# Kernel tuning notes

Hardware: AMD Instinct MI355X
Metric: run time of the kernel (lower is better)

The kernel has to match this reference:

```python
import jax, jax.numpy as jnp
import numpy as np

H = 16      # n_head
DK = 64     # d_k = n_feat // n_head
EPS = 1e-5  # nn.LayerNorm default eps


def _layernorm(x, gamma, beta):
    # LayerNorm over the last (d_k) dim, matching nn.LayerNorm(d_k)
    mu = jnp.mean(x, axis=-1, keepdims=True)
    var = jnp.mean(jnp.square(x - mu), axis=-1, keepdims=True)
    return (x - mu) * jax.lax.rsqrt(var + EPS) * gamma + beta


def setup_inputs() -> dict:
    key = jax.random.key(0)
    ks = jax.random.split(key, 10)
    B, T, D = 4, 1024, 1024
    s = 0.02
    inp = {
        "query": jax.random.normal(ks[0], (B, T, D), dtype=jnp.float32),
        "key":   jax.random.normal(ks[1], (B, T, D), dtype=jnp.float32),
        "value": jax.random.normal(ks[2], (B, T, D), dtype=jnp.float32),
        "mask":  jax.random.randint(ks[3], (B, T, T), 0, 2).astype(bool),
        # projection weights (torch nn.Linear: y = x @ W.T + b)
        "Wq": jax.random.normal(ks[4], (D, D), dtype=jnp.float32) * s,
        "bq": jnp.zeros((D,), dtype=jnp.float32),
        "Wk": jax.random.normal(ks[5], (D, D), dtype=jnp.float32) * s,
        "bk": jnp.zeros((D,), dtype=jnp.float32),
        "Wv": jax.random.normal(ks[6], (D, D), dtype=jnp.float32) * s,
        "bv": jnp.zeros((D,), dtype=jnp.float32),
        "Wo": jax.random.normal(ks[7], (D, D), dtype=jnp.float32) * s,
        "bo": jnp.zeros((D,), dtype=jnp.float32),
        # per-head LayerNorm params over d_k
        "q_gamma": jnp.ones((DK,), dtype=jnp.float32),
        "q_beta":  jnp.zeros((DK,), dtype=jnp.float32),
        "k_gamma": jnp.ones((DK,), dtype=jnp.float32),
        "k_beta":  jnp.zeros((DK,), dtype=jnp.float32),
    }
    return inp


def reference(query, key, value, mask, Wq, bq, Wk, bk, Wv, bv, Wo, bo,
              q_gamma, q_beta, k_gamma, k_beta):
    B, Tq, D = query.shape
    Tk = key.shape[1]
    # forward_qkv: project, split heads, QK-LayerNorm
    q = (query @ Wq.T + bq).reshape(B, Tq, H, DK)
    k = (key   @ Wk.T + bk).reshape(B, Tk, H, DK)
    q = _layernorm(q, q_gamma, q_beta).transpose(0, 2, 1, 3)  # (B,H,Tq,dk)
    k = _layernorm(k, k_gamma, k_beta).transpose(0, 2, 1, 3)  # (B,H,Tk,dk)
    v = (value @ Wv.T + bv).reshape(B, Tk, H, DK).transpose(0, 2, 1, 3)
    # scores scaled by sqrt(d_k)
    scores = jnp.einsum('bhqd,bhkd->bhqk', q, k) / jnp.sqrt(jnp.float32(DK))
    m = mask[:, None]  # (B,1,Tq,Tk) broadcast over heads
    scores = jnp.where(m, jnp.float32(-10000.0), scores)
    attn = jax.nn.softmax(scores, axis=-1)
    attn = jnp.where(m, jnp.float32(0.0), attn)
    # dropout is identity (p=0.0, eval)
    x = jnp.einsum('bhqk,bhkd->bhqd', attn, v)
    x = x.transpose(0, 2, 1, 3).reshape(B, Tq, H * DK)
    return x @ Wo.T + bo
```

## Files before the change

kernel.cpp:

```cpp
#include <hip/hip_runtime.h>
#include <cstdint>
#include <cstddef>

typedef _Float16 half8  __attribute__((ext_vector_type(8)));
typedef _Float16 half4v __attribute__((ext_vector_type(4)));
typedef float    f32x4  __attribute__((ext_vector_type(4)));

__device__ __forceinline__ f32x4 fzero4() {
  f32x4 v; v[0] = v[1] = v[2] = v[3] = 0.0f; return v;
}

__device__ __forceinline__ void gload16(const void* g, void* l) {
  __builtin_amdgcn_global_load_lds(
      (const __attribute__((address_space(1))) unsigned int*)g,
      (__attribute__((address_space(3))) unsigned int*)l, 16, 0, 0);
}

#define MFMA(a, b, c) __builtin_amdgcn_mfma_f32_16x16x32_f16(a, b, c, 0, 0, 0)
#define EXP2(x) __builtin_amdgcn_exp2f(x)

__device__ __forceinline__ float row16_sum(float x) {
#define STEP_(N)                                                         \
  {                                                                      \
    int t_ = __builtin_amdgcn_update_dpp(0, __float_as_int(x), 0x120 | N, \
                                         0xf, 0xf, true);                \
    x = x + __int_as_float(t_);                                          \
  }
  STEP_(8) STEP_(4) STEP_(2) STEP_(1)
#undef STEP_
  return x;
}

struct PrepArgs {
  const float* src[7];
  _Float16*    dst[7];
  const int*   mask;
  unsigned long long* mbits;
};

__global__ __launch_bounds__(256) void prep_kernel(PrepArgs a) {
  const int z = blockIdx.y;
  const int nthr = gridDim.x * blockDim.x;
  const int t0 = blockIdx.x * blockDim.x + threadIdx.x;
  if (z < 3) {
    const float4* __restrict__ s = (const float4*)a.src[z];
    half4v* __restrict__ d = (half4v*)a.dst[z];
    float4 v[8];
#pragma unroll
    for (int k = 0; k < 8; ++k) v[k] = s[t0 + k * nthr];
#pragma unroll
    for (int k = 0; k < 8; ++k) {
      half4v h;
      h[0] = (_Float16)v[k].x; h[1] = (_Float16)v[k].y;
      h[2] = (_Float16)v[k].z; h[3] = (_Float16)v[k].w;
      d[t0 + k * nthr] = h;
    }
  } else if (z < 7) {
    const float4* __restrict__ s = (const float4*)a.src[z];
    half4v* __restrict__ d = (half4v*)a.dst[z];
    float4 v[2];
#pragma unroll
    for (int k = 0; k < 2; ++k) v[k] = s[t0 + k * nthr];
#pragma unroll
    for (int k = 0; k < 2; ++k) {
      half4v h;
      h[0] = (_Float16)v[k].x; h[1] = (_Float16)v[k].y;
      h[2] = (_Float16)v[k].z; h[3] = (_Float16)v[k].w;
      d[t0 + k * nthr] = h;
    }
  } else {
    const int* __restrict__ src = a.mask;
    const unsigned char* __restrict__ s8 = (const unsigned char*)src;
    unsigned long long* __restrict__ dst = a.mbits;
    const int lane = threadIdx.x & 63;
    unsigned probe = 0;
#pragma unroll
    for (int e = 0; e < 16; ++e) probe |= s8[4 * (lane * 16 + e) + 1];
    const bool isbool = __any(probe != 0);

    const int gw = blockIdx.x * 4 + (threadIdx.x >> 6);
    for (int ii = 0; ii < 32; ii += 8) {
      int mv[8];
#pragma unroll
      for (int k = 0; k < 8; ++k) {
        const int word = gw * 32 + ii + k;
        const int t = word & 1023;
        const int kw = (word >> 10) & 15;
        const int b = word >> 14;
        const size_t idx = ((size_t)(b * 1024 + t)) * 1024 + kw * 64 + lane;
        mv[k] = isbool ? (int)s8[idx] : src[idx];
      }
#pragma unroll
      for (int k = 0; k < 8; ++k) {
        unsigned long long bal = __ballot(mv[k] != 0);
        if (lane == 0) dst[gw * 32 + ii + k] = bal;
      }
    }
  }
}

#define SM_SCALE 0.18033688011112042f

__global__ __launch_bounds__(256) void proj_kernel(
    const _Float16* __restrict__ q16, const _Float16* __restrict__ k16,
    const _Float16* __restrict__ v16, const _Float16* __restrict__ w16,
    const float* __restrict__ bq, const float* __restrict__ bk,
    const float* __restrict__ bv,
    const float* __restrict__ qg, const float* __restrict__ qbt,
    const float* __restrict__ kg, const float* __restrict__ kbt,
    _Float16* __restrict__ Qln, _Float16* __restrict__ Kln,
    _Float16* __restrict__ VT) {
  __shared__ _Float16 As[2][128 * 32];
  __shared__ _Float16 Bs[2][128 * 32];

  const int tid = threadIdx.x;
  const int w = tid >> 6, lane = tid & 63, g = lane >> 4, l15 = lane & 15;
  const int flat = blockIdx.x;
  const int swz = (flat & 7) * 96 + (flat >> 3);
  const int bn = swz & 7;
  const int bm = (swz >> 3) & 31;
  const int z = swz >> 8;

  const _Float16* A = (z == 0) ? q16 : ((z == 1) ? k16 : v16);
  const _Float16* W = w16 + (size_t)z * (1024 * 1024);
  const float* bias = (z == 0) ? bq : ((z == 1) ? bk : bv);

  const int wr = w >> 1, wc = w & 1;
  const int lrow16 = lane >> 2;
  const int csw = (((lane & 3) ^ ((lane >> 3) & 3)) << 3);
  const int rslot = (l15 >> 1) & 3;

  f32x4 acc[4][4];
#pragma unroll
  for (int i = 0; i < 4; ++i)
#pragma unroll
    for (int j = 0; j < 4; ++j) acc[i][j] = fzero4();

#define PROJ_STAGE(KT, BUF)                                                 \
  _Pragma("unroll") for (int c = 0; c < 2; ++c) {                           \
    const int row0 = w * 32 + c * 16;                                       \
    gload16(A + (size_t)(bm * 128 + row0 + lrow16) * 1024 + (KT)*32 + csw,  \
            &As[BUF][row0 * 32]);                                           \
    gload16(W + (size_t)(bn * 128 + row0 + lrow16) * 1024 + (KT)*32 + csw,  \
            &Bs[BUF][row0 * 32]);                                           \
  }

#define PROJ_TILE(KT, CUR, NXT, PF)                                         \
  {                                                                         \
    if (PF) { PROJ_STAGE((KT) + 1, NXT) }                                   \
    half8 a[4], b[4];                                                       \
    _Pragma("unroll") for (int mi = 0; mi < 4; ++mi) a[mi] =                \
        *(const half8*)&As[CUR][(wr * 64 + mi * 16 + l15) * 32 +            \
                                ((g ^ rslot) << 3)];                        \
    _Pragma("unroll") for (int nj = 0; nj < 4; ++nj) b[nj] =                \
        *(const half8*)&Bs[CUR][(wc * 64 + nj * 16 + l15) * 32 +            \
                                ((g ^ rslot) << 3)];                        \
    __builtin_amdgcn_s_setprio(1);                                          \
    _Pragma("unroll") for (int mi = 0; mi < 4; ++mi)                        \
        _Pragma("unroll") for (int nj = 0; nj < 4; ++nj) acc[mi][nj] =      \
            MFMA(a[mi], b[nj], acc[mi][nj]);                                \
    __builtin_amdgcn_s_setprio(0);                                          \
    if (PF) {                                                               \
      asm volatile("s_waitcnt vmcnt(0)" ::: "memory");                      \
      __syncthreads();                                                      \
    }                                                                       \
  }

  PROJ_STAGE(0, 0)
  asm volatile("s_waitcnt vmcnt(0)" ::: "memory");
  __syncthreads();
  for (int kt = 0; kt < 32; kt += 2) {
    PROJ_TILE(kt, 0, 1, true);
    PROJ_TILE(kt + 1, 1, 0, (kt + 1) < 31);
  }
#undef PROJ_TILE
#undef PROJ_STAGE

  const int colbase = bn * 128 + wc * 64;
  const int h = colbase >> 6;
  const int rowbase = bm * 128 + wr * 64;

  float biasv[4];
#pragma unroll
  for (int nj = 0; nj < 4; ++nj) biasv[nj] = bias[colbase + nj * 16 + l15];

  if (z < 2) {
    const float* gamma = (z == 0) ? qg : kg;
    const float* beta = (z == 0) ? qbt : kbt;
    const float sc = (z == 0) ? SM_SCALE : 1.0f;
    _Float16* dst = (z == 0) ? Qln : Kln;
    float gam[4], bet[4];
#pragma unroll
    for (int nj = 0; nj < 4; ++nj) {
      gam[nj] = gamma[nj * 16 + l15] * sc;
      bet[nj] = beta[nj * 16 + l15] * sc;
    }
#pragma unroll
    for (int mi = 0; mi < 4; ++mi) {
#pragma unroll
      for (int j = 0; j < 4; ++j) {
        float vals[4], s = 0.f, s2 = 0.f;
#pragma unroll
        for (int nj = 0; nj < 4; ++nj) {
          float v = acc[mi][nj][j] + biasv[nj];
          vals[nj] = v; s += v; s2 += v * v;
        }
        s = row16_sum(s);
        s2 = row16_sum(s2);
        const float mu = s * (1.0f / 64.0f);
        const float var = s2 * (1.0f / 64.0f) - mu * mu;
        const float rs = rsqrtf(var + 1e-5f);
        const int r = rowbase + mi * 16 + g * 4 + j;
        const int b = r >> 10, t = r & 1023;
        _Float16* drow = dst + ((size_t)((b * 16 + h) * 1024 + t)) * 64;
#pragma unroll
        for (int nj = 0; nj < 4; ++nj)
          drow[nj * 16 + l15] =
              (_Float16)((vals[nj] - mu) * rs * gam[nj] + bet[nj]);
      }
    }
  } else {
#pragma unroll
    for (int mi = 0; mi < 4; ++mi) {
      const int r0 = rowbase + mi * 16 + g * 4;
      const int b = r0 >> 10, t0 = r0 & 1023;
#pragma unroll
      for (int nj = 0; nj < 4; ++nj) {
        const int dk = nj * 16 + l15;
        half4v pk;
#pragma unroll
        for (int j = 0; j < 4; ++j)
          pk[j] = (_Float16)(acc[mi][nj][j] + biasv[nj]);
        *(half4v*)&VT[((size_t)((b * 16 + h) * 64 + dk)) * 1024 + t0] = pk;
      }
    }
  }
}

#define PSTR 76

__global__ __launch_bounds__(512) void attn_kernel(
    const _Float16* __restrict__ Qln, const _Float16* __restrict__ Kln,
    const _Float16* __restrict__ VT,
    const unsigned long long* __restrict__ mbits, _Float16* __restrict__ X) {
  __shared__ _Float16 PQ[128 * PSTR];
  __shared__ _Float16 Ks[2][64 * 64];
  __shared__ _Float16 Vs[2][64 * 64];
  __shared__ unsigned long long Mb[2][128];

  const int tid = threadIdx.x;
  const int w = tid >> 6, lane = tid & 63, g = lane >> 4, l15 = lane & 15;
  const int qt = blockIdx.x;
  const int bh = blockIdx.y;
  const int b = bh >> 4, h = bh & 15;

  const int lr8 = lane >> 3;
  const int csw = ((lane & 7) ^ lr8) << 3;

  const _Float16* Qb = Qln + (size_t)bh * 65536;
  const _Float16* Kb = Kln + (size_t)bh * 65536;
  const _Float16* Vb = VT + (size_t)bh * 65536;
  const unsigned long long* mbb = mbits + (size_t)b * 16384 + qt * 128;

  gload16(Qb + (size_t)(qt * 128 + w * 16 + lr8) * 64 + csw, &PQ[(w * 16) * 64]);
  gload16(Qb + (size_t)(qt * 128 + w * 16 + 8 + lr8) * 64 + csw,
          &PQ[(w * 16 + 8) * 64]);
  gload16(Kb + (size_t)(w * 8 + lr8) * 64 + csw, &Ks[0][(w * 8) * 64]);
  gload16(Vb + (size_t)(w * 8 + lr8) * 1024 + csw, &Vs[0][(w * 8) * 64]);
  if (w == 0) gload16(mbb + lane * 2, &Mb[0][0]);
  asm volatile("s_waitcnt vmcnt(0)" ::: "memory");
  __syncthreads();

  const int rsw = (l15 & 7) << 3;
  half8 qf[2];
#pragma unroll
  for (int kk = 0; kk < 2; ++kk)
    qf[kk] = *(const half8*)&PQ[(w * 16 + l15) * 64 + ((kk * 32 + g * 8) ^ rsw)];
  asm volatile("s_waitcnt lgkmcnt(0)" ::: "memory");
  __syncthreads();

  f32x4 o[4];
  float lsum[4];
#pragma unroll
  for (int dn = 0; dn < 4; ++dn) o[dn] = fzero4();
#pragma unroll
  for (int j = 0; j < 4; ++j) lsum[j] = 0.f;

#define ATTN_TILE(KT, CUR, NXT, PF)                                          \
  {                                                                          \
    if (PF) {                                                                \
      gload16(Kb + (size_t)(((KT) + 1) * 64 + w * 8 + lr8) * 64 + csw,       \
              &Ks[NXT][(w * 8) * 64]);                                       \
      gload16(Vb + (size_t)(w * 8 + lr8) * 1024 + ((KT) + 1) * 64 + csw,     \
              &Vs[NXT][(w * 8) * 64]);                                       \
      if (w == 0)                                                            \
        gload16(mbb + (size_t)((KT) + 1) * 1024 + lane * 2, &Mb[NXT][0]);    \
    }                                                                        \
    f32x4 s[4];                                                              \
    _Pragma("unroll") for (int nj = 0; nj < 4; ++nj) s[nj] = fzero4();       \
    _Pragma("unroll") for (int kk = 0; kk < 2; ++kk) {                       \
      half8 qv = qf[kk];                                                     \
      __builtin_amdgcn_s_setprio(1);                                         \
      _Pragma("unroll") for (int nj = 0; nj < 4; ++nj) {                     \
        half8 kf = *(const half8*)&Ks[CUR][(nj * 16 + l15) * 64 +            \
                                          ((kk * 32 + g * 8) ^ rsw)];        \
        s[nj] = MFMA(qv, kf, s[nj]);                                         \
      }                                                                      \
      __builtin_amdgcn_s_setprio(0);                                         \
    }                                                                        \
    _Pragma("unroll") for (int j = 0; j < 4; ++j) {                          \
      const int lrow = w * 16 + g * 4 + j;                                   \
      const unsigned long long mw = Mb[CUR][lrow];                           \
      const unsigned lo = (unsigned)mw, hi = (unsigned)(mw >> 32);           \
      const float p0 = ((lo >> l15) & 1) ? 0.f : EXP2(s[0][j]);              \
      const float p1 = ((lo >> (l15 + 16)) & 1) ? 0.f : EXP2(s[1][j]);       \
      const float p2 = ((hi >> l15) & 1) ? 0.f : EXP2(s[2][j]);              \
      const float p3 = ((hi >> (l15 + 16)) & 1) ? 0.f : EXP2(s[3][j]);       \
      PQ[lrow * PSTR + 0 + l15] = (_Float16)p0;                              \
      PQ[lrow * PSTR + 16 + l15] = (_Float16)p1;                             \
      PQ[lrow * PSTR + 32 + l15] = (_Float16)p2;                             \
      PQ[lrow * PSTR + 48 + l15] = (_Float16)p3;                             \
      lsum[j] += (p0 + p1) + (p2 + p3);                                      \
    }                                                                        \
    _Pragma("unroll") for (int kk = 0; kk < 2; ++kk) {                       \
      half8 pa = *(const half8*)&PQ[(w * 16 + l15) * PSTR + kk * 32 + g * 8];\
      __builtin_amdgcn_s_setprio(1);                                         \
      _Pragma("unroll") for (int dn = 0; dn < 4; ++dn) {                     \
        half8 vf = *(const half8*)&Vs[CUR][(dn * 16 + l15) * 64 +            \
                                           ((kk * 32 + g * 8) ^ rsw)];       \
        o[dn] = MFMA(pa, vf, o[dn]);                                         \
      }                                                                      \
      __builtin_amdgcn_s_setprio(0);                                         \
    }                                                                        \
    if (PF) {                                                                \
      asm volatile("s_waitcnt vmcnt(0)" ::: "memory");                       \
      __syncthreads();                                                       \
    }                                                                        \
  }

  for (int kt = 0; kt < 16; kt += 2) {
    ATTN_TILE(kt, 0, 1, true);
    ATTN_TILE(kt + 1, 1, 0, (kt + 1) < 15);
  }
#undef ATTN_TILE

#pragma unroll
  for (int j = 0; j < 4; ++j) {
    const int t = qt * 128 + w * 16 + g * 4 + j;
    const float inv = 1.0f / row16_sum(lsum[j]);
    _Float16* xrow = X + ((size_t)(b * 1024 + t)) * 1024 + h * 64;
#pragma unroll
    for (int dn = 0; dn < 4; ++dn)
      xrow[dn * 16 + l15] = (_Float16)(o[dn][j] * inv);
  }
}

__global__ __launch_bounds__(512) void ogemm_kernel(
    const _Float16* __restrict__ Xin, const _Float16* __restrict__ Wo16,
    const float* __restrict__ bo, float* __restrict__ out) {
  __shared__ _Float16 As[2][128 * 32];
  __shared__ _Float16 Bs[2][128 * 32];

  const int tid = threadIdx.x;
  const int w = tid >> 6, lane = tid & 63, g = lane >> 4, l15 = lane & 15;
  const int flat = blockIdx.x;
  const int swz = (flat & 7) * 32 + (flat >> 3);
  const int bn = swz & 7;
  const int bm = swz >> 3;
  const int wr = w >> 2, wc = w & 3;
  const int lrow16 = lane >> 2;
  const int csw = (((lane & 3) ^ ((lane >> 3) & 3)) << 3);
  const int rslot = (l15 >> 1) & 3;

  f32x4 acc[4][2];
#pragma unroll
  for (int i = 0; i < 4; ++i)
#pragma unroll
    for (int j = 0; j < 2; ++j) acc[i][j] = fzero4();

#define OG_STAGE(KT, BUF)                                                   \
  {                                                                         \
    const int row0 = w * 16;                                                \
    gload16(Xin + (size_t)(bm * 128 + row0 + lrow16) * 1024 + (KT)*32 + csw,\
            &As[BUF][row0 * 32]);                                           \
    gload16(Wo16 + (size_t)(bn * 128 + row0 + lrow16) * 1024 + (KT)*32 +    \
                csw,                                                        \
            &Bs[BUF][row0 * 32]);                                           \
  }

#define OG_TILE(KT, CUR, NXT, PF)                                           \
  {                                                                         \
    if (PF) { OG_STAGE((KT) + 1, NXT) }                                     \
    half8 a[4], b[2];                                                       \
    _Pragma("unroll") for (int mi = 0; mi < 4; ++mi) a[mi] =                \
        *(const half8*)&As[CUR][(wr * 64 + mi * 16 + l15) * 32 +            \
                                ((g ^ rslot) << 3)];                        \
    _Pragma("unroll") for (int nj = 0; nj < 2; ++nj) b[nj] =                \
        *(const half8*)&Bs[CUR][(wc * 32 + nj * 16 + l15) * 32 +            \
                                ((g ^ rslot) << 3)];                        \
    __builtin_amdgcn_s_setprio(1);                                          \
    _Pragma("unroll") for (int mi = 0; mi < 4; ++mi)                        \
        _Pragma("unroll") for (int nj = 0; nj < 2; ++nj) acc[mi][nj] =      \
            MFMA(a[mi], b[nj], acc[mi][nj]);                                \
    __builtin_amdgcn_s_setprio(0);                                          \
    if (PF) {                                                               \
      asm volatile("s_waitcnt vmcnt(0)" ::: "memory");                      \
      __syncthreads();                                                      \
    }                                                                       \
  }

  OG_STAGE(0, 0)
  asm volatile("s_waitcnt vmcnt(0)" ::: "memory");
  __syncthreads();
  for (int kt = 0; kt < 32; kt += 2) {
    OG_TILE(kt, 0, 1, true);
    OG_TILE(kt + 1, 1, 0, (kt + 1) < 31);
  }
#undef OG_TILE
#undef OG_STAGE

  const int colbase = bn * 128 + wc * 32;
  const int rowbase = bm * 128 + wr * 64;
  float biasv[2];
#pragma unroll
  for (int nj = 0; nj < 2; ++nj) biasv[nj] = bo[colbase + nj * 16 + l15];
#pragma unroll
  for (int mi = 0; mi < 4; ++mi)
#pragma unroll
    for (int nj = 0; nj < 2; ++nj)
#pragma unroll
      for (int j = 0; j < 4; ++j) {
        const int r = rowbase + mi * 16 + g * 4 + j;
        out[(size_t)r * 1024 + colbase + nj * 16 + l15] =
            acc[mi][nj][j] + biasv[nj];
      }
}

extern "C" void kernel_launch(void* const* d_in, const int* in_sizes, int n_in,
                              void* d_out, int out_size, void* d_ws,
                              size_t ws_size, hipStream_t stream) {
  const float* query = (const float*)d_in[0];
  const float* key = (const float*)d_in[1];
  const float* value = (const float*)d_in[2];
  const int* mask = (const int*)d_in[3];
  const float* Wq = (const float*)d_in[4];
  const float* bq = (const float*)d_in[5];
  const float* Wk = (const float*)d_in[6];
  const float* bk = (const float*)d_in[7];
  const float* Wv = (const float*)d_in[8];
  const float* bv = (const float*)d_in[9];
  const float* Wo = (const float*)d_in[10];
  const float* bo = (const float*)d_in[11];
  const float* qg = (const float*)d_in[12];
  const float* qb = (const float*)d_in[13];
  const float* kg = (const float*)d_in[14];
  const float* kb = (const float*)d_in[15];
  float* out = (float*)d_out;

  const size_t M4 = (size_t)4 * 1024 * 1024;
  const size_t M1 = (size_t)1024 * 1024;
  _Float16* q16 = (_Float16*)d_ws;
  _Float16* k16 = q16 + M4;
  _Float16* v16 = k16 + M4;
  _Float16* w16 = v16 + M4;
  _Float16* Qln = w16 + M4;
  _Float16* Kln = Qln + M4;
  _Float16* VTp = Kln + M4;
  _Float16* X = VTp + M4;
  unsigned long long* mbits = (unsigned long long*)(X + M4);

  PrepArgs pa;
  pa.src[0] = query; pa.src[1] = key; pa.src[2] = value;
  pa.src[3] = Wq; pa.src[4] = Wk; pa.src[5] = Wv; pa.src[6] = Wo;
  pa.dst[0] = q16; pa.dst[1] = k16; pa.dst[2] = v16;
  pa.dst[3] = w16; pa.dst[4] = w16 + M1; pa.dst[5] = w16 + 2 * M1;
  pa.dst[6] = w16 + 3 * M1;
  pa.mask = mask;
  pa.mbits = mbits;

  prep_kernel<<<dim3(512, 8), 256, 0, stream>>>(pa);
  proj_kernel<<<dim3(768), 256, 0, stream>>>(
      q16, k16, v16, w16, bq, bk, bv, qg, qb, kg, kb, Qln, Kln, VTp);
  attn_kernel<<<dim3(8, 64), 512, 0, stream>>>(Qln, Kln, VTp, mbits, X);
  ogemm_kernel<<<dim3(256), 512, 0, stream>>>(X, w16 + 3 * M1, bo, out);
}
```

Baseline: 130.3 us.

## Triple-buffer GEMM K-loops with partial vmcnt waits and retile output GEMM

Both projection GEMMs move from double buffering with full vmcnt(0) drains to a three-stage LDS ring that keeps one tile of loads in flight, using partial waitcnt and raw s_barrier. The output GEMM is retiled to 128x64 tiles with a K-step of 64, 256 threads and 512 blocks, using a new XOR swizzle. The attention grid is transposed so consecutive blocks walk across batch-heads rather than query tiles. This trades more LDS per block for better overlap of global loads with MFMA work and better occupancy in the last GEMM.

```diff
diff --git a/kernel.cpp b/kernel.cpp
--- a/kernel.cpp
+++ b/kernel.cpp
@@ -18,6 +18,8 @@
 
 #define MFMA(a, b, c) __builtin_amdgcn_mfma_f32_16x16x32_f16(a, b, c, 0, 0, 0)
 #define EXP2(x) __builtin_amdgcn_exp2f(x)
+#define WAITV(N) asm volatile("s_waitcnt vmcnt(" #N ")" ::: "memory")
+#define BAR() __builtin_amdgcn_s_barrier()
 
 __device__ __forceinline__ float row16_sum(float x) {
 #define STEP_(N)                                                         \
@@ -110,8 +112,8 @@
     const float* __restrict__ kg, const float* __restrict__ kbt,
     _Float16* __restrict__ Qln, _Float16* __restrict__ Kln,
     _Float16* __restrict__ VT) {
-  __shared__ _Float16 As[2][128 * 32];
-  __shared__ _Float16 Bs[2][128 * 32];
+  __shared__ _Float16 As[3][128 * 32];
+  __shared__ _Float16 Bs[3][128 * 32];
 
   const int tid = threadIdx.x;
   const int w = tid >> 6, lane = tid & 63, g = lane >> 4, l15 = lane & 15;
@@ -145,9 +147,8 @@
             &Bs[BUF][row0 * 32]);                                           \
   }
 
-#define PROJ_TILE(KT, CUR, NXT, PF)                                         \
+#define PROJ_COMP(CUR)                                                      \
   {                                                                         \
-    if (PF) { PROJ_STAGE((KT) + 1, NXT) }                                   \
     half8 a[4], b[4];                                                       \
     _Pragma("unroll") for (int mi = 0; mi < 4; ++mi) a[mi] =                \
         *(const half8*)&As[CUR][(wr * 64 + mi * 16 + l15) * 32 +            \
@@ -160,20 +161,22 @@
         _Pragma("unroll") for (int nj = 0; nj < 4; ++nj) acc[mi][nj] =      \
             MFMA(a[mi], b[nj], acc[mi][nj]);                                \
     __builtin_amdgcn_s_setprio(0);                                          \
-    if (PF) {                                                               \
-      asm volatile("s_waitcnt vmcnt(0)" ::: "memory");                      \
-      __syncthreads();                                                      \
-    }                                                                       \
   }
 
   PROJ_STAGE(0, 0)
-  asm volatile("s_waitcnt vmcnt(0)" ::: "memory");
-  __syncthreads();
-  for (int kt = 0; kt < 32; kt += 2) {
-    PROJ_TILE(kt, 0, 1, true);
-    PROJ_TILE(kt + 1, 1, 0, (kt + 1) < 31);
-  }
-#undef PROJ_TILE
+  PROJ_STAGE(1, 1)
+  WAITV(4);
+  BAR();
+  for (int t = 0; t < 30; t += 3) {
+    PROJ_STAGE(t + 2, 2) PROJ_COMP(0) WAITV(4); BAR();
+    PROJ_STAGE(t + 3, 0) PROJ_COMP(1) WAITV(4); BAR();
+    PROJ_STAGE(t + 4, 1) PROJ_COMP(2) WAITV(4); BAR();
+  }
+  PROJ_COMP(0)
+  WAITV(0);
+  BAR();
+  PROJ_COMP(1)
+#undef PROJ_COMP
 #undef PROJ_STAGE
 
   const int colbase = bn * 128 + wc * 64;
@@ -250,8 +253,8 @@
 
   const int tid = threadIdx.x;
   const int w = tid >> 6, lane = tid & 63, g = lane >> 4, l15 = lane & 15;
-  const int qt = blockIdx.x;
-  const int bh = blockIdx.y;
+  const int qt = blockIdx.y;
+  const int bh = blockIdx.x;
   const int b = bh >> 4, h = bh & 15;
 
   const int lr8 = lane >> 3;
@@ -355,22 +358,23 @@
   }
 }
 
-__global__ __launch_bounds__(512) void ogemm_kernel(
+__global__ __launch_bounds__(256) void ogemm_kernel(
     const _Float16* __restrict__ Xin, const _Float16* __restrict__ Wo16,
     const float* __restrict__ bo, float* __restrict__ out) {
-  __shared__ _Float16 As[2][128 * 32];
-  __shared__ _Float16 Bs[2][128 * 32];
+  __shared__ _Float16 As[3][128 * 64];
+  __shared__ _Float16 Bs[3][64 * 64];
 
   const int tid = threadIdx.x;
   const int w = tid >> 6, lane = tid & 63, g = lane >> 4, l15 = lane & 15;
   const int flat = blockIdx.x;
-  const int swz = (flat & 7) * 32 + (flat >> 3);
-  const int bn = swz & 7;
-  const int bm = swz >> 3;
-  const int wr = w >> 2, wc = w & 3;
-  const int lrow16 = lane >> 2;
-  const int csw = (((lane & 3) ^ ((lane >> 3) & 3)) << 3);
-  const int rslot = (l15 >> 1) & 3;
+  const int swz = (flat & 7) * 64 + (flat >> 3);
+  const int bn = swz & 15;
+  const int bm = swz >> 4;
+  const int wr = w >> 1, wc = w & 1;
+  const int srow = (w << 3) + (lane >> 3);
+  const int lr8 = lane >> 3;
+  const int csw = ((lane & 7) ^ lr8) << 3;
+  const int rsw = (l15 & 7) << 3;
 
   f32x4 acc[4][2];
 #pragma unroll
@@ -380,46 +384,51 @@
 
 #define OG_STAGE(KT, BUF)                                                   \
   {                                                                         \
-    const int row0 = w * 16;                                                \
-    gload16(Xin + (size_t)(bm * 128 + row0 + lrow16) * 1024 + (KT)*32 + csw,\
-            &As[BUF][row0 * 32]);                                           \
-    gload16(Wo16 + (size_t)(bn * 128 + row0 + lrow16) * 1024 + (KT)*32 +    \
-                csw,                                                        \
-            &Bs[BUF][row0 * 32]);                                           \
-  }
-
-#define OG_TILE(KT, CUR, NXT, PF)                                           \
-  {                                                                         \
-    if (PF) { OG_STAGE((KT) + 1, NXT) }                                     \
+    _Pragma("unroll") for (int r = 0; r < 4; ++r) {                         \
+      gload16(Xin + (size_t)(bm * 128 + r * 32 + srow) * 1024 + (KT)*64 +   \
+                  csw,                                                      \
+              &As[BUF][(r * 32 + (w << 3)) * 64]);                          \
+    }                                                                       \
+    _Pragma("unroll") for (int c = 0; c < 2; ++c) {                         \
+      gload16(Wo16 + (size_t)(bn * 64 + w * 16 + c * 8 + lr8) * 1024 +      \
+                  (KT)*64 + csw,                                            \
+              &Bs[BUF][(w * 16 + c * 8) * 64]);                             \
+    }                                                                       \
+  }
+
+#define OG_COMP(CUR)                                                        \
+  _Pragma("unroll") for (int kk = 0; kk < 2; ++kk) {                        \
     half8 a[4], b[2];                                                       \
     _Pragma("unroll") for (int mi = 0; mi < 4; ++mi) a[mi] =                \
-        *(const half8*)&As[CUR][(wr * 64 + mi * 16 + l15) * 32 +            \
-                                ((g ^ rslot) << 3)];                        \
+        *(const half8*)&As[CUR][(wr * 64 + mi * 16 + l15) * 64 +            \
+                                ((kk * 32 + g * 8) ^ rsw)];                 \
     _Pragma("unroll") for (int nj = 0; nj < 2; ++nj) b[nj] =                \
-        *(const half8*)&Bs[CUR][(wc * 32 + nj * 16 + l15) * 32 +            \
-                                ((g ^ rslot) << 3)];                        \
+        *(const half8*)&Bs[CUR][(wc * 32 + nj * 16 + l15) * 64 +            \
+                                ((kk * 32 + g * 8) ^ rsw)];                 \
     __builtin_amdgcn_s_setprio(1);                                          \
     _Pragma("unroll") for (int mi = 0; mi < 4; ++mi)                        \
         _Pragma("unroll") for (int nj = 0; nj < 2; ++nj) acc[mi][nj] =      \
             MFMA(a[mi], b[nj], acc[mi][nj]);                                \
     __builtin_amdgcn_s_setprio(0);                                          \
-    if (PF) {                                                               \
-      asm volatile("s_waitcnt vmcnt(0)" ::: "memory");                      \
-      __syncthreads();                                                      \
-    }                                                                       \
   }
 
   OG_STAGE(0, 0)
-  asm volatile("s_waitcnt vmcnt(0)" ::: "memory");
-  __syncthreads();
-  for (int kt = 0; kt < 32; kt += 2) {
-    OG_TILE(kt, 0, 1, true);
-    OG_TILE(kt + 1, 1, 0, (kt + 1) < 31);
-  }
-#undef OG_TILE
+  OG_STAGE(1, 1)
+  WAITV(6);
+  BAR();
+  for (int t = 0; t < 12; t += 3) {
+    OG_STAGE(t + 2, 2) OG_COMP(0) WAITV(6); BAR();
+    OG_STAGE(t + 3, 0) OG_COMP(1) WAITV(6); BAR();
+    OG_STAGE(t + 4, 1) OG_COMP(2) WAITV(6); BAR();
+  }
+  OG_STAGE(14, 2) OG_COMP(0) WAITV(6); BAR();
+  OG_STAGE(15, 0) OG_COMP(1) WAITV(6); BAR();
+  OG_COMP(2) WAITV(0); BAR();
+  OG_COMP(0)
+#undef OG_COMP
 #undef OG_STAGE
 
-  const int colbase = bn * 128 + wc * 32;
+  const int colbase = bn * 64 + wc * 32;
   const int rowbase = bm * 128 + wr * 64;
   float biasv[2];
 #pragma unroll
@@ -481,6 +490,6 @@
   prep_kernel<<<dim3(512, 8), 256, 0, stream>>>(pa);
   proj_kernel<<<dim3(768), 256, 0, stream>>>(
       q16, k16, v16, w16, bq, bk, bv, qg, qb, kg, kb, Qln, Kln, VTp);
-  attn_kernel<<<dim3(8, 64), 512, 0, stream>>>(Qln, Kln, VTp, mbits, X);
-  ogemm_kernel<<<dim3(256), 512, 0, stream>>>(X, w16 + 3 * M1, bo, out);
-}
+  attn_kernel<<<dim3(64, 8), 512, 0, stream>>>(Qln, Kln, VTp, mbits, X);
+  ogemm_kernel<<<dim3(512), 256, 0, stream>>>(X, w16 + 3 * M1, bo, out);
+}
```

After: 128.4 us. No clear change (-1.5%).
